# Kernel tuning notes

Measured on AMD Instinct MI355X. Metric: run time of the kernel, lower is better.

The kernel has to match this reference:

```python
import jax, jax.numpy as jnp
import numpy as np

N = 50000      # num nodes
E0 = 300000    # raw random edges (symmetrized + self loops -> E = 2*E0 + N = 650000)
F = 128        # input feature dim
H = 4          # num_heads
A = 32         # attention_size
O = 64         # out_size
TOL = 1e-5


def setup_inputs() -> dict:
    key = jax.random.key(0)
    k1, k2, k3 = jax.random.split(key, 3)
    rng = np.random.default_rng(0)
    r = rng.integers(0, N, E0)
    c = rng.integers(0, N, E0)
    loops = np.arange(N)
    # symmetrize so the per-head adjacency (values depend only on endpoints) is
    # self-adjoint, and add self-loops so every node has nonzero degree.
    row = jnp.asarray(np.concatenate([r, c, loops]), dtype=jnp.int32)
    col = jnp.asarray(np.concatenate([c, r, loops]), dtype=jnp.int32)
    features = jax.random.normal(k1, (N, F), jnp.float32)
    w_attn = jax.random.normal(k2, (F, H * A), jnp.float32) / np.sqrt(F)
    b_attn = jnp.zeros((H * A,), jnp.float32)
    w_out = jax.random.normal(k3, (F, H * O), jnp.float32) / np.sqrt(F)
    b_out = jnp.zeros((H * O,), jnp.float32)
    epsilon_sig_inv = jnp.full((H,), -2.0, jnp.float32)  # hk.get_parameter init
    return dict(row=row, col=col, features=features, w_attn=w_attn, b_attn=b_attn,
                w_out=w_out, b_out=b_out, epsilon_sig_inv=epsilon_sig_inv)


def reference(row, col, features, w_attn, b_attn, w_out, b_out, epsilon_sig_inv):
    n = features.shape[0]
    # per-edge sigmoid attention: [E, H]
    a = (features @ w_attn + b_attn).reshape(n, H, A)
    attn = jax.nn.sigmoid(jnp.einsum('eha,eha->eh', a[row], a[col]))
    eps = jax.nn.sigmoid(epsilon_sig_inv)  # [H]
    f = (features @ w_out + b_out).reshape(n, H, O)

    # symmetric normalization D^{-1/2} A D^{-1/2}, per head
    deg = jax.ops.segment_sum(attn, row, num_segments=n)  # [N, H]
    safe = jnp.where(deg > 0, deg, 1.0)
    inv_sqrt = jnp.where(deg > 0, jax.lax.rsqrt(safe), 0.0)
    vals = attn * inv_sqrt[row] * inv_sqrt[col]  # [E, H]

    def solve_head(vals_h, eps_h, f_h):
        # (I - (1 - eps) * A_norm)^{-1} @ f_h via CG (self-adjoint inverse)
        scale = 1.0 - eps_h

        def matvec(x):  # x: [N, O]
            ax = jax.ops.segment_sum(vals_h[:, None] * x[col], row, num_segments=n)
            return x - scale * ax

        y, _ = jax.scipy.sparse.linalg.cg(matvec, f_h, tol=TOL)
        return y

    out = jax.vmap(solve_head, in_axes=(1, 0, 1), out_axes=1)(vals, eps, f)  # [N, H, O]
    return out.mean(axis=1)  # sum(out) / num_heads
```

## Files before the change

### kernel.cpp

```cpp
#include <hip/hip_runtime.h>
#include <hip/hip_bf16.h>
#include <hip/hip_fp16.h>
#include <math.h>

#define NIT 9

typedef _Float16 f16x8 __attribute__((ext_vector_type(8)));
typedef float    f32x4 __attribute__((ext_vector_type(4)));

__global__ void conv_w_kernel(const float* __restrict__ w_attn, const float* __restrict__ b_attn,
                              const float* __restrict__ w_out,  const float* __restrict__ b_out,
                              __half* __restrict__ wt, float* __restrict__ bias)
{
    int tid = blockIdx.x * blockDim.x + threadIdx.x;
    if (tid >= 384 * 128) return;
    int c = tid >> 7, k = tid & 127;
    float v = (c < 128) ? w_attn[(size_t)k * 128 + c] : w_out[(size_t)k * 256 + (c - 128)];
    wt[tid] = __float2half(v);
    if (k == 0) bias[c] = (c < 128) ? b_attn[c] : b_out[c - 128];
}

__device__ __forceinline__ f16x8 cvt8(const float* __restrict__ p)
{
    float4 v0 = *(const float4*)p;
    float4 v1 = *(const float4*)(p + 4);
    f16x8 r;
    r[0] = (_Float16)v0.x; r[1] = (_Float16)v0.y;
    r[2] = (_Float16)v0.z; r[3] = (_Float16)v0.w;
    r[4] = (_Float16)v1.x; r[5] = (_Float16)v1.y;
    r[6] = (_Float16)v1.z; r[7] = (_Float16)v1.w;
    return r;
}

__global__ __launch_bounds__(256) void mfma_gemm_kernel(
    const float* __restrict__ feat, const __half* __restrict__ wt,
    const float* __restrict__ bias,
    __half* __restrict__ a_half, __half* __restrict__ bh, int n)
{
    int w = threadIdx.x >> 6;
    int lane = threadIdx.x & 63;
    int m0 = blockIdx.x * 32;
    int colbase = w * 96;
    int mrow = lane & 15, kgrp = lane >> 4;
    int r0c = m0 + mrow;      if (r0c > n - 1) r0c = n - 1;
    int r1c = m0 + 16 + mrow; if (r1c > n - 1) r1c = n - 1;
    f32x4 acc[2][6] = {};
    #pragma unroll
    for (int ks = 0; ks < 4; ++ks) {
        int k0 = ks * 32 + kgrp * 8;
        f16x8 a0 = cvt8(feat + (size_t)r0c * 128 + k0);
        f16x8 a1 = cvt8(feat + (size_t)r1c * 128 + k0);
        #pragma unroll
        for (int ct = 0; ct < 6; ++ct) {
            int gcol = colbase + ct * 16 + mrow;
            f16x8 b = *(const f16x8*)(wt + (size_t)gcol * 128 + k0);
            acc[0][ct] = __builtin_amdgcn_mfma_f32_16x16x32_f16(a0, b, acc[0][ct], 0, 0, 0);
            acc[1][ct] = __builtin_amdgcn_mfma_f32_16x16x32_f16(a1, b, acc[1][ct], 0, 0, 0);
        }
    }
    #pragma unroll
    for (int rt = 0; rt < 2; ++rt) {
        #pragma unroll
        for (int ct = 0; ct < 6; ++ct) {
            int gcol = colbase + ct * 16 + mrow;
            float bv = bias[gcol];
            #pragma unroll
            for (int j = 0; j < 4; ++j) {
                int grow = m0 + rt * 16 + kgrp * 4 + j;
                if (grow >= n) continue;
                float v = acc[rt][ct][j] + bv;
                if (gcol < 128) a_half[(size_t)grow * 128 + gcol] = __float2half(v);
                else            bh[(size_t)grow * 256 + (gcol - 128)] = __float2half(v);
            }
        }
    }
}

__global__ void edge_attn_sym_kernel(const int* __restrict__ row, const int* __restrict__ col,
                                     const __half* __restrict__ a_half, float* __restrict__ attn,
                                     int* __restrict__ cnt, int E0, int nu)
{
    int gtid = blockIdx.x * blockDim.x + threadIdx.x;
    int g = gtid >> 4;
    int lane = gtid & 15;
    int u0 = 2 * g;
    if (u0 >= nu) return;
    int u1 = u0 + 1;
    bool has1 = (u1 < nu);
    int e0 = (u0 < E0) ? u0 : u0 + E0;
    int e1 = has1 ? ((u1 < E0) ? u1 : u1 + E0) : e0;
    int r0 = row[e0], c0 = col[e0];
    int r1 = row[e1], c1 = col[e1];
    float4 av0 = ((const float4*)(a_half + (size_t)r0 * 128))[lane];
    float4 bv0 = ((const float4*)(a_half + (size_t)c0 * 128))[lane];
    float4 av1 = ((const float4*)(a_half + (size_t)r1 * 128))[lane];
    float4 bv1 = ((const float4*)(a_half + (size_t)c1 * 128))[lane];
    float p0 = 0.f, p1 = 0.f;
    {
        const __half2* a2 = (const __half2*)&av0;
        const __half2* b2 = (const __half2*)&bv0;
        #pragma unroll
        for (int q = 0; q < 4; ++q) {
            float2 fa = __half22float2(a2[q]);
            float2 fb = __half22float2(b2[q]);
            p0 += fa.x * fb.x + fa.y * fb.y;
        }
    }
    {
        const __half2* a2 = (const __half2*)&av1;
        const __half2* b2 = (const __half2*)&bv1;
        #pragma unroll
        for (int q = 0; q < 4; ++q) {
            float2 fa = __half22float2(a2[q]);
            float2 fb = __half22float2(b2[q]);
            p1 += fa.x * fb.x + fa.y * fb.y;
        }
    }
    p0 += __shfl_xor(p0, 1); p0 += __shfl_xor(p0, 2);
    p1 += __shfl_xor(p1, 1); p1 += __shfl_xor(p1, 2);
    int h = lane >> 2, j = lane & 3;
    if (j == 0) {
        float sg0 = 1.0f / (1.0f + __expf(-p0));
        attn[(size_t)e0*4 + h] = sg0;
        if (u0 < E0) attn[(size_t)(e0 + E0)*4 + h] = sg0;
        if (has1) {
            float sg1 = 1.0f / (1.0f + __expf(-p1));
            attn[(size_t)e1*4 + h] = sg1;
            if (u1 < E0) attn[(size_t)(e1 + E0)*4 + h] = sg1;
        }
    }
    if (lane == 0) {
        if (u0 < E0) { atomicAdd(&cnt[r0], 1); atomicAdd(&cnt[c0], 1); }
        if (has1 && u1 < E0) { atomicAdd(&cnt[r1], 1); atomicAdd(&cnt[c1], 1); }
    }
}

__global__ __launch_bounds__(1024) void scanA_kernel(const int* __restrict__ cnt,
                                                     int* __restrict__ local,
                                                     int* __restrict__ bsum, int n)
{
    __shared__ int s[1024];
    int t = threadIdx.x;
    int i = blockIdx.x * 1024 + t;
    int v = (i < n) ? cnt[i] : 0;
    s[t] = v;
    __syncthreads();
    for (int off = 1; off < 1024; off <<= 1) {
        int tmp = (t >= off) ? s[t - off] : 0;
        __syncthreads();
        s[t] += tmp;
        __syncthreads();
    }
    if (i < n) local[i] = s[t] - v;
    if (t == 1023) bsum[blockIdx.x] = s[t];
}

__global__ __launch_bounds__(1024) void scanB_kernel(int* __restrict__ bsum,
                                                     int* __restrict__ rowp,
                                                     int nb, int n)
{
    __shared__ int s[1024];
    int t = threadIdx.x;
    int v = (t < nb) ? bsum[t] : 0;
    s[t] = v;
    __syncthreads();
    for (int off = 1; off < 1024; off <<= 1) {
        int tmp = (t >= off) ? s[t - off] : 0;
        __syncthreads();
        s[t] += tmp;
        __syncthreads();
    }
    if (t < nb) bsum[t] = s[t] - v;
    if (t == nb - 1) rowp[n] = s[t];
}

__global__ void scanC_kernel(int* __restrict__ local_nxt, const int* __restrict__ bsum,
                             int* __restrict__ rowp, int n)
{
    int i = blockIdx.x * blockDim.x + threadIdx.x;
    if (i >= n) return;
    int v = local_nxt[i] + bsum[i >> 10];
    rowp[i] = v;
    local_nxt[i] = v;
}

__global__ void scatter_kernel(const int* __restrict__ row, const int* __restrict__ col,
                               int* __restrict__ next, int* __restrict__ col_s,
                               int* __restrict__ perm, int ne2)
{
    int e = blockIdx.x * blockDim.x + threadIdx.x;
    if (e >= ne2) return;
    int pos = atomicAdd(&next[row[e]], 1);
    col_s[pos] = col[e];
    perm[pos] = e;
}

__global__ __launch_bounds__(256) void deg_csr_kernel(
    const int* __restrict__ perm, const float* __restrict__ attn,
    const int* __restrict__ rowp, float* __restrict__ deg, int E0, int n)
{
    int wid = threadIdx.x >> 6;
    int lane = threadIdx.x & 63;
    int i = blockIdx.x * 4 + wid;
    if (i >= n) return;
    int start = rowp[i], end = rowp[i + 1];
    int h = lane & 3;
    float s = 0.f;
    for (int p = start + (lane >> 2); p < end; p += 16) {
        int e = perm[p];
        s += attn[(size_t)e * 4 + h];
    }
    s += __shfl_xor(s, 4);
    s += __shfl_xor(s, 8);
    s += __shfl_xor(s, 16);
    s += __shfl_xor(s, 32);
    if (lane < 4) {
        s += attn[(size_t)(2 * E0 + i) * 4 + h];
        deg[(size_t)i * 4 + h] = s;
    }
}

__global__ void isq_kernel(const float* __restrict__ deg, float* __restrict__ isq, int nh)
{
    int i = blockIdx.x * blockDim.x + threadIdx.x;
    if (i >= nh) return;
    float dg = deg[i];
    isq[i] = (dg > 0.f) ? rsqrtf(dg) : 0.f;
}

__global__ void coeff_kernel(const float* __restrict__ eps_inv, float* __restrict__ coeff)
{
    int h = threadIdx.x;
    if (h >= 4) return;
    float eps = 1.0f / (1.0f + expf(-eps_inv[h]));
    float s = 1.0f - eps;
    coeff[h] = s;
    float sigma2 = 2.0f / s;
    float rho = s;
    for (int k = 0; k < NIT; ++k) {
        float rhon = 1.0f / (sigma2 - rho);
        coeff[4 + k*4 + h] = rhon * rho;
        coeff[4 + NIT*4 + k*4 + h] = 2.0f * rhon / s;
        rho = rhon;
    }
}

__global__ void vals_kernel(const int* __restrict__ perm, const int* __restrict__ row,
                            const int* __restrict__ col, const float* __restrict__ attn,
                            const float* __restrict__ isq, const float* __restrict__ coeff,
                            __half* __restrict__ valsh, int ne2)
{
    int p = blockIdx.x * blockDim.x + threadIdx.x;
    if (p >= ne2) return;
    int e = perm[p];
    int r0 = row[e], c0 = col[e];
    #pragma unroll
    for (int h = 0; h < 4; ++h)
        valsh[(size_t)p*4 + h] = __float2half(
            coeff[h] * attn[(size_t)e*4 + h]
            * isq[(size_t)r0*4 + h] * isq[(size_t)c0*4 + h]);
}

__global__ void dw_kernel(const float* __restrict__ attn, const float* __restrict__ isq,
                          const float* __restrict__ coeff, float* __restrict__ dw,
                          int E0, int nh)
{
    int tid = blockIdx.x * blockDim.x + threadIdx.x;
    if (tid >= nh) return;
    int i = tid >> 2, h = tid & 3;
    float q = isq[tid];
    dw[tid] = coeff[h] * attn[(size_t)(2*E0 + i)*4 + h] * q * q;
}

__device__ __forceinline__ void gather_row(
    const __half2* __restrict__ x2, const __half* __restrict__ valsh,
    const int* __restrict__ col_s, int start, int end, int lane, int h,
    float& a0, float& a1, float& a2, float& a3)
{
    int p = start;
    for (; p + 8 <= end; p += 8) {
        float w[8];
        uint2 u[8];
        #pragma unroll
        for (int q = 0; q < 8; ++q) {
            int c = col_s[p + q];
            w[q] = __half2float(valsh[(size_t)(p + q) * 4 + h]);
            u[q] = *(const uint2*)(x2 + (size_t)c * 128 + lane * 2);
        }
        #pragma unroll
        for (int q = 0; q < 8; ++q) {
            float2 f0 = __half22float2(*(__half2*)&u[q].x);
            float2 f1 = __half22float2(*(__half2*)&u[q].y);
            a0 += w[q] * f0.x; a1 += w[q] * f0.y;
            a2 += w[q] * f1.x; a3 += w[q] * f1.y;
        }
    }
    int len = end - p;
    {
        float w[8];
        uint2 u[8];
        #pragma unroll
        for (int q = 0; q < 8; ++q) {
            if (q < len) {
                int c = col_s[p + q];
                w[q] = __half2float(valsh[(size_t)(p + q) * 4 + h]);
                u[q] = *(const uint2*)(x2 + (size_t)c * 128 + lane * 2);
            }
        }
        #pragma unroll
        for (int q = 0; q < 8; ++q) {
            if (q < len) {
                float2 f0 = __half22float2(*(__half2*)&u[q].x);
                float2 f1 = __half22float2(*(__half2*)&u[q].y);
                a0 += w[q] * f0.x; a1 += w[q] * f0.y;
                a2 += w[q] * f1.x; a3 += w[q] * f1.y;
            }
        }
    }
}

template <bool FINAL>
__global__ __launch_bounds__(256) void cheb_kernel(
    const __half* __restrict__ xch, const __half* __restrict__ xph,
    const __half* __restrict__ bh, const float* __restrict__ dw,
    __half* __restrict__ xnh, float* __restrict__ out,
    const __half* __restrict__ valsh, const int* __restrict__ col_s,
    const int* __restrict__ row_ptr, const float* __restrict__ coeff, int k, int n)
{
    int wid = threadIdx.x >> 6;
    int lane = threadIdx.x & 63;
    int i = blockIdx.x * 4 + wid;
    if (i >= n) return;
    int h = lane >> 4;
    const __half2* x2 = (const __half2*)xch;
    int start = row_ptr[i], end = row_ptr[i + 1];
    float a0 = 0.f, a1 = 0.f, a2 = 0.f, a3 = 0.f;
    gather_row(x2, valsh, col_s, start, end, lane, h, a0, a1, a2, a3);
    size_t idx2 = (size_t)i * 128 + lane * 2;
    float2 xc0 = __half22float2(x2[idx2]);
    float2 xc1 = __half22float2(x2[idx2 + 1]);
    float2 xp0 = xph ? __half22float2(((const __half2*)xph)[idx2])     : make_float2(0.f, 0.f);
    float2 xp1 = xph ? __half22float2(((const __half2*)xph)[idx2 + 1]) : make_float2(0.f, 0.f);
    float2 bv0 = __half22float2(((const __half2*)bh)[idx2]);
    float2 bv1 = __half22float2(((const __half2*)bh)[idx2 + 1]);
    float dwv = dw[(size_t)i * 4 + h];
    float r0 = bv0.x - xc0.x + a0 + dwv * xc0.x;
    float r1 = bv0.y - xc0.y + a1 + dwv * xc0.y;
    float r2 = bv1.x - xc1.x + a2 + dwv * xc1.x;
    float r3 = bv1.y - xc1.y + a3 + dwv * xc1.y;
    float c1v = coeff[4 + k*4 + h];
    float c2v = coeff[4 + NIT*4 + k*4 + h];
    float v0 = xc0.x + c1v * (xc0.x - xp0.x) + c2v * r0;
    float v1 = xc0.y + c1v * (xc0.y - xp0.y) + c2v * r1;
    float v2 = xc1.x + c1v * (xc1.x - xp1.x) + c2v * r2;
    float v3 = xc1.y + c1v * (xc1.y - xp1.y) + c2v * r3;
    if (FINAL) {
        v0 += __shfl_xor(v0, 16); v0 += __shfl_xor(v0, 32);
        v1 += __shfl_xor(v1, 16); v1 += __shfl_xor(v1, 32);
        v2 += __shfl_xor(v2, 16); v2 += __shfl_xor(v2, 32);
        v3 += __shfl_xor(v3, 16); v3 += __shfl_xor(v3, 32);
        if (lane < 16) {
            float4 o = make_float4(0.25f*v0, 0.25f*v1, 0.25f*v2, 0.25f*v3);
            ((float4*)out)[(size_t)i * 16 + lane] = o;
        }
    } else {
        __half2* xo = (__half2*)xnh;
        xo[idx2]     = __floats2half2_rn(v0, v1);
        xo[idx2 + 1] = __floats2half2_rn(v2, v3);
    }
}

__global__ void fill_kernel(float* __restrict__ out, int sz, float v)
{
    int i = blockIdx.x * blockDim.x + threadIdx.x;
    if (i < sz) out[i] = v;
}

extern "C" void kernel_launch(void* const* d_in, const int* in_sizes, int n_in,
                              void* d_out, int out_size, void* d_ws, size_t ws_size,
                              hipStream_t stream)
{
    const int*   row     = (const int*)d_in[0];
    const int*   col     = (const int*)d_in[1];
    const float* feat    = (const float*)d_in[2];
    const float* w_attn  = (const float*)d_in[3];
    const float* b_attn  = (const float*)d_in[4];
    const float* w_out   = (const float*)d_in[5];
    const float* b_out   = (const float*)d_in[6];
    const float* eps_inv = (const float*)d_in[7];
    float* out = (float*)d_out;

    int n  = in_sizes[2] / 128;
    int ne = in_sizes[0];
    int E0 = (ne - n) / 2;
    int ne2 = 2 * E0;
    int nb = (n + 1023) / 1024;

    char* wsb = (char*)d_ws;
    size_t off = 0;
    auto alloc = [&](size_t bytes) -> void* {
        void* p = wsb + off;
        off += (bytes + 255) & ~(size_t)255;
        return p;
    };
    __half* a_half = (__half*)alloc((size_t)n * 128 * 2);
    __half* bh     = (__half*)alloc((size_t)n * 256 * 2);
    __half* hA     = (__half*)alloc((size_t)n * 256 * 2);
    __half* hB     = (__half*)alloc((size_t)n * 256 * 2);
    __half* wt     = (__half*)alloc((size_t)384 * 128 * 2);
    float*  bias   = (float*)alloc((size_t)384 * 4);
    __half* valsh  = (__half*)alloc((size_t)ne2 * 4 * 2);
    float*  deg    = (float*)alloc((size_t)n * 4 * 4);
    float*  isq    = (float*)alloc((size_t)n * 4 * 4);
    float*  dw     = (float*)alloc((size_t)n * 4 * 4);
    int*    rowp   = (int*)alloc((size_t)(n + 1) * 4);
    int*    col_s  = (int*)alloc((size_t)ne2 * 4);
    int*    bsum   = (int*)alloc((size_t)((nb + 63) & ~63) * 4);
    float*  coeff  = (float*)alloc((size_t)(4 + 8 * NIT) * 4);

    int*   perm = (int*)hA;
    int*   cnt  = (int*)((char*)hA + (((size_t)ne2*4 + 255) & ~(size_t)255));
    int*   nxt  = cnt + ((n + 64) & ~63);
    float* attn = (float*)hB;

    if (off > ws_size) {
        fill_kernel<<<(out_size + 255) / 256, 256, 0, stream>>>(out, out_size, 1e9f);
        return;
    }

    hipMemsetAsync(cnt, 0, (size_t)n * 4, stream);

    conv_w_kernel<<<(384 * 128 + 255) / 256, 256, 0, stream>>>(w_attn, b_attn,
                                                               w_out, b_out, wt, bias);
    mfma_gemm_kernel<<<(n + 31) / 32, 256, 0, stream>>>(feat, wt, bias, a_half, bh, n);
    coeff_kernel<<<1, 64, 0, stream>>>(eps_inv, coeff);

    int nu = E0 + n;
    int ngroups = (nu + 1) / 2;
    int ublocks = (ngroups * 16 + 255) / 256;
    edge_attn_sym_kernel<<<ublocks, 256, 0, stream>>>(row, col, a_half, attn,
                                                      cnt, E0, nu);

    scanA_kernel<<<nb, 1024, 0, stream>>>(cnt, nxt, bsum, n);
    scanB_kernel<<<1, 1024, 0, stream>>>(bsum, rowp, nb, n);
    scanC_kernel<<<(n + 255) / 256, 256, 0, stream>>>(nxt, bsum, rowp, n);
    scatter_kernel<<<(ne2 + 255) / 256, 256, 0, stream>>>(row, col, nxt, col_s, perm, ne2);
    deg_csr_kernel<<<(n + 3) / 4, 256, 0, stream>>>(perm, attn, rowp, deg, E0, n);
    isq_kernel<<<(n * 4 + 255) / 256, 256, 0, stream>>>(deg, isq, n * 4);
    vals_kernel<<<(ne2 + 255) / 256, 256, 0, stream>>>(perm, row, col, attn, isq,
                                                       coeff, valsh, ne2);
    dw_kernel<<<(n * 4 + 255) / 256, 256, 0, stream>>>(attn, isq, coeff, dw, E0, n * 4);

    int cgrid = (n + 3) / 4;
    cheb_kernel<false><<<cgrid, 256, 0, stream>>>(
        bh, nullptr, bh, dw, hA, nullptr, valsh, col_s, rowp, coeff, 0, n);
    cheb_kernel<false><<<cgrid, 256, 0, stream>>>(
        hA, bh, bh, dw, hB, nullptr, valsh, col_s, rowp, coeff, 1, n);
    for (int k = 2; k < NIT; ++k) {
        __half* cur = (k & 1) ? hA : hB;
        __half* prv = (k & 1) ? hB : hA;
        if (k == NIT - 1)
            cheb_kernel<true><<<cgrid, 256, 0, stream>>>(
                cur, prv, bh, dw, nullptr, out, valsh, col_s, rowp, coeff, k, n);
        else
            cheb_kernel<false><<<cgrid, 256, 0, stream>>>(
                cur, prv, bh, dw, prv, nullptr, valsh, col_s, rowp, coeff, k, n);
    }
}
```

Before: 677.2 us.

## Sort rows by degree for Chebyshev SpMM load balance, shrink blocks

Adds a degree histogram, scan and scatter that produce a row permutation grouping nodes by degree. Each Chebyshev iteration kernel then processes rows in that order, so wavefronts in a block see similar edge counts. Blocks shrink from 4 to 2 waves. The bias load becomes a nontemporal load. Three extra small kernels are added, and the permuted row order loses the sequential locality of x and out accesses.

```diff
diff --git a/kernel.cpp b/kernel.cpp
--- a/kernel.cpp
+++ b/kernel.cpp
@@ -2,11 +2,13 @@
 #include <hip/hip_bf16.h>
 #include <hip/hip_fp16.h>
 #include <math.h>
+#include <string.h>
 
 #define NIT 9
 
 typedef _Float16 f16x8 __attribute__((ext_vector_type(8)));
 typedef float    f32x4 __attribute__((ext_vector_type(4)));
+typedef unsigned int u32x2 __attribute__((ext_vector_type(2)));
 
 __global__ void conv_w_kernel(const float* __restrict__ w_attn, const float* __restrict__ b_attn,
                               const float* __restrict__ w_out,  const float* __restrict__ b_out,
@@ -195,6 +197,43 @@
     perm[pos] = e;
 }
 
+__global__ void dhist_kernel(const int* __restrict__ rowp, int* __restrict__ dh, int n)
+{
+    int i = blockIdx.x * blockDim.x + threadIdx.x;
+    if (i >= n) return;
+    int d = rowp[i + 1] - rowp[i];
+    if (d > 255) d = 255;
+    atomicAdd(&dh[d], 1);
+}
+
+__global__ __launch_bounds__(256) void dscan_kernel(const int* __restrict__ dh,
+                                                    int* __restrict__ doff)
+{
+    __shared__ int s[256];
+    int t = threadIdx.x;
+    int v = dh[t];
+    s[t] = v;
+    __syncthreads();
+    for (int o = 1; o < 256; o <<= 1) {
+        int tmp = (t >= o) ? s[t - o] : 0;
+        __syncthreads();
+        s[t] += tmp;
+        __syncthreads();
+    }
+    doff[t] = s[t] - v;
+}
+
+__global__ void dscatter_kernel(const int* __restrict__ rowp, int* __restrict__ doff,
+                                int* __restrict__ rsort, int n)
+{
+    int i = blockIdx.x * blockDim.x + threadIdx.x;
+    if (i >= n) return;
+    int d = rowp[i + 1] - rowp[i];
+    if (d > 255) d = 255;
+    int pos = atomicAdd(&doff[d], 1);
+    rsort[pos] = i;
+}
+
 __global__ __launch_bounds__(256) void deg_csr_kernel(
     const int* __restrict__ perm, const float* __restrict__ attn,
     const int* __restrict__ rowp, float* __restrict__ deg, int E0, int n)
@@ -320,17 +359,19 @@
 }
 
 template <bool FINAL>
-__global__ __launch_bounds__(256) void cheb_kernel(
+__global__ __launch_bounds__(128) void cheb_kernel(
     const __half* __restrict__ xch, const __half* __restrict__ xph,
     const __half* __restrict__ bh, const float* __restrict__ dw,
     __half* __restrict__ xnh, float* __restrict__ out,
     const __half* __restrict__ valsh, const int* __restrict__ col_s,
-    const int* __restrict__ row_ptr, const float* __restrict__ coeff, int k, int n)
+    const int* __restrict__ row_ptr, const int* __restrict__ rsort,
+    const float* __restrict__ coeff, int k, int n)
 {
     int wid = threadIdx.x >> 6;
     int lane = threadIdx.x & 63;
-    int i = blockIdx.x * 4 + wid;
-    if (i >= n) return;
+    int gw = blockIdx.x * 2 + wid;
+    if (gw >= n) return;
+    int i = rsort[gw];
     int h = lane >> 4;
     const __half2* x2 = (const __half2*)xch;
     int start = row_ptr[i], end = row_ptr[i + 1];
@@ -341,8 +382,10 @@
     float2 xc1 = __half22float2(x2[idx2 + 1]);
     float2 xp0 = xph ? __half22float2(((const __half2*)xph)[idx2])     : make_float2(0.f, 0.f);
     float2 xp1 = xph ? __half22float2(((const __half2*)xph)[idx2 + 1]) : make_float2(0.f, 0.f);
-    float2 bv0 = __half22float2(((const __half2*)bh)[idx2]);
-    float2 bv1 = __half22float2(((const __half2*)bh)[idx2 + 1]);
+    u32x2 ub = __builtin_nontemporal_load((const u32x2*)bh + ((size_t)i * 64 + lane));
+    unsigned ub0 = ub[0], ub1 = ub[1];
+    float2 bv0 = __half22float2(*reinterpret_cast<__half2*>(&ub0));
+    float2 bv1 = __half22float2(*reinterpret_cast<__half2*>(&ub1));
     float dwv = dw[(size_t)i * 4 + h];
     float r0 = bv0.x - xc0.x + a0 + dwv * xc0.x;
     float r1 = bv0.y - xc0.y + a1 + dwv * xc0.y;
@@ -416,6 +459,9 @@
     int*    rowp   = (int*)alloc((size_t)(n + 1) * 4);
     int*    col_s  = (int*)alloc((size_t)ne2 * 4);
     int*    bsum   = (int*)alloc((size_t)((nb + 63) & ~63) * 4);
+    int*    rsort  = (int*)alloc((size_t)n * 4);
+    int*    dh     = (int*)alloc(256 * 4);
+    int*    doff   = (int*)alloc(256 * 4);
     float*  coeff  = (float*)alloc((size_t)(4 + 8 * NIT) * 4);
 
     int*   perm = (int*)hA;
@@ -429,6 +475,7 @@
     }
 
     hipMemsetAsync(cnt, 0, (size_t)n * 4, stream);
+    hipMemsetAsync(dh, 0, 256 * 4, stream);
 
     conv_w_kernel<<<(384 * 128 + 255) / 256, 256, 0, stream>>>(w_attn, b_attn,
                                                                w_out, b_out, wt, bias);
@@ -445,25 +492,30 @@
     scanB_kernel<<<1, 1024, 0, stream>>>(bsum, rowp, nb, n);
     scanC_kernel<<<(n + 255) / 256, 256, 0, stream>>>(nxt, bsum, rowp, n);
     scatter_kernel<<<(ne2 + 255) / 256, 256, 0, stream>>>(row, col, nxt, col_s, perm, ne2);
+
+    dhist_kernel<<<(n + 255) / 256, 256, 0, stream>>>(rowp, dh, n);
+    dscan_kernel<<<1, 256, 0, stream>>>(dh, doff);
+    dscatter_kernel<<<(n + 255) / 256, 256, 0, stream>>>(rowp, doff, rsort, n);
+
     deg_csr_kernel<<<(n + 3) / 4, 256, 0, stream>>>(perm, attn, rowp, deg, E0, n);
     isq_kernel<<<(n * 4 + 255) / 256, 256, 0, stream>>>(deg, isq, n * 4);
     vals_kernel<<<(ne2 + 255) / 256, 256, 0, stream>>>(perm, row, col, attn, isq,
                                                        coeff, valsh, ne2);
     dw_kernel<<<(n * 4 + 255) / 256, 256, 0, stream>>>(attn, isq, coeff, dw, E0, n * 4);
 
-    int cgrid = (n + 3) / 4;
-    cheb_kernel<false><<<cgrid, 256, 0, stream>>>(
-        bh, nullptr, bh, dw, hA, nullptr, valsh, col_s, rowp, coeff, 0, n);
-    cheb_kernel<false><<<cgrid, 256, 0, stream>>>(
-        hA, bh, bh, dw, hB, nullptr, valsh, col_s, rowp, coeff, 1, n);
+    int cgrid = (n + 1) / 2;
+    cheb_kernel<false><<<cgrid, 128, 0, stream>>>(
+        bh, nullptr, bh, dw, hA, nullptr, valsh, col_s, rowp, rsort, coeff, 0, n);
+    cheb_kernel<false><<<cgrid, 128, 0, stream>>>(
+        hA, bh, bh, dw, hB, nullptr, valsh, col_s, rowp, rsort, coeff, 1, n);
     for (int k = 2; k < NIT; ++k) {
         __half* cur = (k & 1) ? hA : hB;
         __half* prv = (k & 1) ? hB : hA;
         if (k == NIT - 1)
-            cheb_kernel<true><<<cgrid, 256, 0, stream>>>(
-                cur, prv, bh, dw, nullptr, out, valsh, col_s, rowp, coeff, k, n);
+            cheb_kernel<true><<<cgrid, 128, 0, stream>>>(
+                cur, prv, bh, dw, nullptr, out, valsh, col_s, rowp, rsort, coeff, k, n);
         else
-            cheb_kernel<false><<<cgrid, 256, 0, stream>>>(
-                cur, prv, bh, dw, prv, nullptr, valsh, col_s, rowp, coeff, k, n);
-    }
-}
+            cheb_kernel<false><<<cgrid, 128, 0, stream>>>(
+                cur, prv, bh, dw, prv, nullptr, valsh, col_s, rowp, rsort, coeff, k, n);
+    }
+}
```

Result: slower. 1.029 ms (+51.9%).
